# Performance work log

Measured on AMD Instinct MI355X. Metric: run time of the kernel, lower is better.

The kernel has to match this reference:

```python
import jax, jax.numpy as jnp
import numpy as np

DIM = 3072          # model dim
H = 24              # num heads (q == kv heads here)
DH = 128            # head dim
EPS = 1e-6
SCALE = 1.0 / float(np.sqrt(DH))
S_IMG, S_TXT, B = 2048, 256, 1


def _rmsnorm(x, w):
    # per-head RMSNorm over last (head_dim) axis
    return x * jax.lax.rsqrt(jnp.mean(x * x, axis=-1, keepdims=True) + EPS) * w


def _rope_non_neox(x, cos, sin):
    # x: [B,S,H,DH]; cos/sin: [S,DH/2]; interleaved (non-neox) rotation
    x1 = x[..., 0::2]
    x2 = x[..., 1::2]
    c = cos[None, :, None, :]
    s = sin[None, :, None, :]
    o1 = x1 * c - x2 * s
    o2 = x2 * c + x1 * s
    return jnp.stack([o1, o2], axis=-1).reshape(x.shape)


def setup_inputs() -> dict:
    key = jax.random.key(0)
    ks = jax.random.split(key, 16)
    hidden_states = jax.random.normal(ks[0], (B, S_IMG, DIM), jnp.float32)
    encoder_hidden_states = jax.random.normal(ks[1], (B, S_TXT, DIM), jnp.float32)
    vid_ang = jax.random.uniform(ks[2], (S_IMG, DH // 2), jnp.float32) * (2 * np.pi)
    txt_ang = jax.random.uniform(ks[3], (S_TXT, DH // 2), jnp.float32) * (2 * np.pi)
    w = 0.02
    return {
        "hidden_states": hidden_states,
        "encoder_hidden_states": encoder_hidden_states,
        "vid_cos": jnp.cos(vid_ang), "vid_sin": jnp.sin(vid_ang),
        "txt_cos": jnp.cos(txt_ang), "txt_sin": jnp.sin(txt_ang),
        "w_qkv": jax.random.normal(ks[4], (DIM, 3 * H * DH), jnp.float32) * w,
        "b_qkv": jnp.zeros((3 * H * DH,), jnp.float32),
        "w_add_qkv": jax.random.normal(ks[5], (DIM, 3 * H * DH), jnp.float32) * w,
        "b_add_qkv": jnp.zeros((3 * H * DH,), jnp.float32),
        "norm_q_w": jnp.ones((DH,), jnp.float32),
        "norm_k_w": jnp.ones((DH,), jnp.float32),
        "norm_aq_w": jnp.ones((DH,), jnp.float32),
        "norm_ak_w": jnp.ones((DH,), jnp.float32),
        "w_out": jax.random.normal(ks[6], (H * DH, DIM), jnp.float32) * w,
        "b_out": jnp.zeros((DIM,), jnp.float32),
        "w_add_out": jax.random.normal(ks[7], (H * DH, DIM), jnp.float32) * w,
        "b_add_out": jnp.zeros((DIM,), jnp.float32),
    }


def reference(hidden_states, encoder_hidden_states, vid_cos, vid_sin,
              txt_cos, txt_sin, w_qkv, b_qkv, w_add_qkv, b_add_qkv,
              norm_q_w, norm_k_w, norm_aq_w, norm_ak_w,
              w_out, b_out, w_add_out, b_add_out):
    qs = H * DH
    # fused QKV projections
    img_qkv = hidden_states @ w_qkv + b_qkv                  # [B,Si,3*H*DH]
    txt_qkv = encoder_hidden_states @ w_add_qkv + b_add_qkv  # [B,St,3*H*DH]

    def split_heads(qkv, S):
        q, k, v = qkv[..., :qs], qkv[..., qs:2 * qs], qkv[..., 2 * qs:]
        shp = (qkv.shape[0], S, H, DH)
        return q.reshape(shp), k.reshape(shp), v.reshape(shp)

    img_q, img_k, img_v = split_heads(img_qkv, S_IMG)
    txt_q, txt_k, txt_v = split_heads(txt_qkv, S_TXT)

    # per-head RMSNorm on q/k
    img_q = _rmsnorm(img_q, norm_q_w)
    img_k = _rmsnorm(img_k, norm_k_w)
    txt_q = _rmsnorm(txt_q, norm_aq_w)
    txt_k = _rmsnorm(txt_k, norm_ak_w)

    # non-neox RoPE on both query and key
    img_q = _rope_non_neox(img_q, vid_cos, vid_sin)
    img_k = _rope_non_neox(img_k, vid_cos, vid_sin)
    txt_q = _rope_non_neox(txt_q, txt_cos, txt_sin)
    txt_k = _rope_non_neox(txt_k, txt_cos, txt_sin)

    # joint text|image attention (text first), non-causal SDPA
    q = jnp.concatenate([txt_q, img_q], axis=1)  # [B,S,H,DH]
    k = jnp.concatenate([txt_k, img_k], axis=1)
    v = jnp.concatenate([txt_v, img_v], axis=1)

    scores = jnp.einsum('bqhd,bkhd->bhqk', q, k) * SCALE
    probs = jax.nn.softmax(scores, axis=-1)
    attn = jnp.einsum('bhqk,bkhd->bqhd', probs, v)           # [B,S,H,DH]
    attn = attn.reshape(attn.shape[0], attn.shape[1], H * DH)

    txt_attn = attn[:, :S_TXT, :]
    img_attn = attn[:, S_TXT:, :]
    img_out = img_attn @ w_out + b_out
    txt_out = txt_attn @ w_add_out + b_add_out
    return (img_out, txt_out)
```

## Files before the change

kernel.cpp:

```cpp
#include <hip/hip_runtime.h>

typedef unsigned short u16;
typedef __attribute__((ext_vector_type(8))) short bf16x8;
typedef __attribute__((ext_vector_type(4))) float f32x4;
typedef __attribute__((ext_vector_type(16))) float f32x16;

#define H_    24
#define DH_   128
#define DIM_  3072
#define NQKV_ 9216
#define SIMG_ 2048
#define STXT_ 256
#define SQ_   2304
#define SL_   0.1275258646912204f

__device__ __forceinline__ float bf2f(u16 h) {
  union { unsigned u; float f; } x; x.u = ((unsigned)h) << 16; return x.f;
}
__device__ __forceinline__ u16 f2bf(float f) {
  union { float f; unsigned u; } x; x.f = f;
  unsigned r = x.u + 0x7FFFu + ((x.u >> 16) & 1u);
  return (u16)(r >> 16);
}
__device__ __forceinline__ unsigned cvt_pk_bf16(float lo, float hi) {
  unsigned r;
  asm("v_cvt_pk_bf16_f32 %0, %1, %2" : "=v"(r) : "v"(lo), "v"(hi));
  return r;
}

__device__ __forceinline__ void gld16(const u16* g, u16* l) {
  __builtin_amdgcn_global_load_lds(
      (const __attribute__((address_space(1))) unsigned*)g,
      (__attribute__((address_space(3))) unsigned*)l, 16, 0, 0);
}

__global__ __launch_bounds__(256) void k_f2b2(const float* __restrict__ in0,
                                              u16* __restrict__ out0, int n0,
                                              const float* __restrict__ in1,
                                              u16* __restrict__ out1, int n1) {
  int i = (blockIdx.x * 256 + threadIdx.x) * 4;
  const float* in = in0;
  u16* out = out0;
  int n = n0;
  if (i >= n0) { i -= n0; in = in1; out = out1; n = n1; }
  if (i < n) {
    float4 v = *(const float4*)(in + i);
    ushort4 o;
    o.x = f2bf(v.x); o.y = f2bf(v.y); o.z = f2bf(v.z); o.w = f2bf(v.w);
    *(ushort4*)(out + i) = o;
  }
}

__global__ __launch_bounds__(256) void k_transpose2(const float* __restrict__ in0,
                                                    u16* __restrict__ out0,
                                                    const float* __restrict__ in1,
                                                    u16* __restrict__ out1,
                                                    int R, int C) {
  __shared__ __align__(16) u16 tile[64][72];
  const float* in = blockIdx.z ? in1 : in0;
  u16* out = blockIdx.z ? out1 : out0;
  const int t = threadIdx.x;
  const int tx = t & 15, ty = t >> 4;
  const int bc = blockIdx.x * 64, br = blockIdx.y * 64;
#pragma unroll
  for (int i = 0; i < 4; ++i) {
    const int r = ty + i * 16;
    float4 v = *(const float4*)(in + (size_t)(br + r) * C + bc + tx * 4);
    ushort4 o;
    o.x = f2bf(v.x); o.y = f2bf(v.y); o.z = f2bf(v.z); o.w = f2bf(v.w);
    *(ushort4*)&tile[r][tx * 4] = o;
  }
  __syncthreads();
#pragma unroll
  for (int i = 0; i < 4; ++i) {
    const int c = ty + i * 16;
    ushort4 v;
    v.x = tile[tx * 4 + 0][c];
    v.y = tile[tx * 4 + 1][c];
    v.z = tile[tx * 4 + 2][c];
    v.w = tile[tx * 4 + 3][c];
    *(ushort4*)(out + (size_t)(bc + c) * R + br + tx * 4) = v;
  }
}

template <bool F32OUT>
__global__ __launch_bounds__(256) void k_gemm_bt2(const u16* __restrict__ A0,
                                                  const u16* __restrict__ Bt0,
                                                  const float* __restrict__ bias0,
                                                  void* __restrict__ C0,
                                                  int M0,
                                                  const u16* __restrict__ A1,
                                                  const u16* __restrict__ Bt1,
                                                  const float* __restrict__ bias1,
                                                  void* __restrict__ C1,
                                                  int M1,
                                                  int N, int K, int nblk0) {
  __shared__ __align__(16) u16 As[2][128 * 32];
  __shared__ __align__(16) u16 Bs[2][128 * 32];
  const int t = threadIdx.x, w = t >> 6, l = t & 63;
  const int lr = l & 15, lg = l >> 4;
  const int wr = w >> 1, wc = w & 1;

  const u16 *A, *Bt;
  const float* bias;
  void* Cv;
  int M, wg, nwg;
  if ((int)blockIdx.x < nblk0) {
    A = A0; Bt = Bt0; bias = bias0; Cv = C0; M = M0;
    wg = blockIdx.x; nwg = nblk0;
  } else {
    A = A1; Bt = Bt1; bias = bias1; Cv = C1; M = M1;
    wg = blockIdx.x - nblk0; nwg = gridDim.x - nblk0;
  }
  const int nbm = M >> 7;
  if ((nwg & 7) == 0) {
    const int c = nwg >> 3;
    wg = (wg & 7) * c + (wg >> 3);
  }
  const int bm = (wg % nbm) * 128, bn = (wg / nbm) * 128;

  f32x4 acc[4][4];
#pragma unroll
  for (int i = 0; i < 4; ++i)
#pragma unroll
    for (int j = 0; j < 4; ++j) acc[i][j] = (f32x4){0.f, 0.f, 0.f, 0.f};

  const u16* Ag = A + (size_t)(bm + (t >> 2)) * K + (t & 3) * 8;
  const u16* Bg = Bt + (size_t)(bn + (t >> 2)) * K + (t & 3) * 8;

#define GSTAGE(buf)                                        \
  do {                                                     \
    gld16(Ag, &As[buf][t * 8]);                            \
    gld16(Ag + (size_t)64 * K, &As[buf][t * 8 + 2048]);    \
    gld16(Bg, &Bs[buf][t * 8]);                            \
    gld16(Bg + (size_t)64 * K, &Bs[buf][t * 8 + 2048]);    \
    Ag += 32; Bg += 32;                                    \
  } while (0)

  GSTAGE(0);
  const int nt = K >> 5;
  for (int tile = 0; tile < nt; ++tile) {
    const int cur = tile & 1;
    if (tile + 1 < nt) {
      GSTAGE(cur ^ 1);
      asm volatile("s_waitcnt vmcnt(4)" ::: "memory");
    } else {
      asm volatile("s_waitcnt vmcnt(0)" ::: "memory");
    }
    __builtin_amdgcn_s_barrier();
    bf16x8 af[4], bfr[4];
#pragma unroll
    for (int i = 0; i < 4; ++i)
      af[i] = *(const bf16x8*)&As[cur][(wr * 64 + i * 16 + lr) * 32 + lg * 8];
#pragma unroll
    for (int j = 0; j < 4; ++j)
      bfr[j] = *(const bf16x8*)&Bs[cur][(wc * 64 + j * 16 + lr) * 32 + lg * 8];
#pragma unroll
    for (int i = 0; i < 4; ++i)
#pragma unroll
      for (int j = 0; j < 4; ++j)
        acc[i][j] = __builtin_amdgcn_mfma_f32_16x16x32_bf16(af[i], bfr[j], acc[i][j], 0, 0, 0);
    __builtin_amdgcn_s_barrier();
  }
#undef GSTAGE

#pragma unroll
  for (int j = 0; j < 4; ++j) {
    const int col = bn + wc * 64 + j * 16 + lr;
    const float bv = bias[col];
#pragma unroll
    for (int i = 0; i < 4; ++i) {
      const int row = bm + wr * 64 + i * 16 + lg * 4;
#pragma unroll
      for (int r = 0; r < 4; ++r) {
        const float v = acc[i][j][r] + bv;
        if constexpr (F32OUT)
          ((float*)Cv)[(size_t)(row + r) * N + col] = v;
        else
          ((u16*)Cv)[(size_t)(row + r) * N + col] = f2bf(v);
      }
    }
  }
}

__global__ __launch_bounds__(256) void k_prep(
    const u16* __restrict__ img_qkv, const u16* __restrict__ txt_qkv,
    const float* __restrict__ vid_cos, const float* __restrict__ vid_sin,
    const float* __restrict__ txt_cos, const float* __restrict__ txt_sin,
    const float* __restrict__ nq, const float* __restrict__ nk,
    const float* __restrict__ naq, const float* __restrict__ nak,
    u16* __restrict__ Qb, u16* __restrict__ Kb, u16* __restrict__ Vt) {
  __shared__ __align__(16) u16 tile[64][136];
  const int t = threadIdx.x;
  if (blockIdx.x < (SQ_ / 64) * H_) {
    const int h = blockIdx.x / (SQ_ / 64), sb = blockIdx.x % (SQ_ / 64);
    {
      const int row = t >> 2, cc = (t & 3) * 32;
      const int s = sb * 64 + row;
      const u16* src = (s < STXT_) ? (txt_qkv + (size_t)s * NQKV_)
                                   : (img_qkv + (size_t)(s - STXT_) * NQKV_);
      src += 2 * DIM_ + h * DH_ + cc;
#pragma unroll
      for (int u = 0; u < 4; ++u) {
        uint4 a = *(const uint4*)(src + u * 8);
        *(uint4*)&tile[row][cc + u * 8] = a;
      }
    }
    __syncthreads();
    {
      const int w = t >> 6, lane = t & 63;
#pragma unroll 4
      for (int dd = 0; dd < 32; ++dd) {
        const int d = w * 32 + dd;
        const int m = (d & 7) << 3;
        const u16 v = tile[lane][d];
        Vt[((size_t)h * DH_ + d) * SQ_ + sb * 64 + (lane ^ m)] = v;
      }
    }
    return;
  }
  const int wid = (blockIdx.x - (SQ_ / 64) * H_) * 4 + (t >> 6);
  const int lane = t & 63;
  const int h = wid % H_, s = wid / H_;

  const u16* src;
  const float *cp, *sp, *qw, *kw;
  if (s < STXT_) {
    src = txt_qkv + (size_t)s * NQKV_;
    cp = txt_cos + s * 64; sp = txt_sin + s * 64;
    qw = naq; kw = nak;
  } else {
    const int si = s - STXT_;
    src = img_qkv + (size_t)si * NQKV_;
    cp = vid_cos + si * 64; sp = vid_sin + si * 64;
    qw = nq; kw = nk;
  }
  const float c = cp[lane], sn = sp[lane];
  const size_t drow = ((size_t)h * SQ_ + s) * DH_;

  {
    ushort2 p = *(const ushort2*)(src + h * DH_ + 2 * lane);
    float x1 = bf2f(p.x), x2 = bf2f(p.y);
    float ss = x1 * x1 + x2 * x2;
#pragma unroll
    for (int m = 1; m < 64; m <<= 1) ss += __shfl_xor(ss, m);
    const float rr = rsqrtf(ss * (1.0f / 128.0f) + 1e-6f);
    const float xn1 = x1 * rr * qw[2 * lane];
    const float xn2 = x2 * rr * qw[2 * lane + 1];
    ushort2 o; o.x = f2bf(xn1 * c - xn2 * sn); o.y = f2bf(xn2 * c + xn1 * sn);
    *(ushort2*)(Qb + drow + 2 * lane) = o;
  }
  {
    ushort2 p = *(const ushort2*)(src + DIM_ + h * DH_ + 2 * lane);
    float x1 = bf2f(p.x), x2 = bf2f(p.y);
    float ss = x1 * x1 + x2 * x2;
#pragma unroll
    for (int m = 1; m < 64; m <<= 1) ss += __shfl_xor(ss, m);
    const float rr = rsqrtf(ss * (1.0f / 128.0f) + 1e-6f);
    const float xn1 = x1 * rr * kw[2 * lane];
    const float xn2 = x2 * rr * kw[2 * lane + 1];
    ushort2 o; o.x = f2bf(xn1 * c - xn2 * sn); o.y = f2bf(xn2 * c + xn1 * sn);
    const int col = (2 * lane) ^ ((s & 7) << 3);
    *(ushort2*)(Kb + drow + col) = o;
  }
}

__global__ __launch_bounds__(256, 2) void k_attn(const u16* __restrict__ Qb,
                                                 const u16* __restrict__ Kb,
                                                 const u16* __restrict__ Vt,
                                                 u16* __restrict__ attnb) {
  __shared__ __align__(16) u16 Ks[2][64 * 128];
  __shared__ __align__(16) u16 Vs[2][128 * 64];
  const int t = threadIdx.x, w = t >> 6, l = t & 63;
  const int lo = l & 31, hi = l >> 5;

  const int bid = blockIdx.x;
  const int xcd = bid & 7, jj = bid >> 3;
  const int h = xcd * 3 + jj / 18;
  const int qb = jj % 18;

  const int q0 = qb * 128 + w * 32;
  const size_t head = (size_t)h * SQ_ * DH_;

  bf16x8 qf[8];
  {
    const u16* qp = Qb + head + (size_t)(q0 + lo) * DH_ + hi * 8;
#pragma unroll
    for (int ks = 0; ks < 8; ++ks) qf[ks] = *(const bf16x8*)(qp + ks * 16);
  }
  f32x16 oacc[4];
#pragma unroll
  for (int dt = 0; dt < 4; ++dt)
#pragma unroll
    for (int i = 0; i < 16; ++i) oacc[dt][i] = 0.f;
  float mrun = -1e30f, lrun = 0.f;

  const u16* kg0 = Kb + head + (size_t)(t >> 4) * DH_ + (t & 15) * 8;
  const u16* vg0 = Vt + head + (size_t)(t >> 3) * SQ_ + (t & 7) * 8;
  const int swz = (lo & 7) << 3;

#define STAGE(buf, kt)                                                   \
  do {                                                                   \
    const u16* kg_ = kg0 + (size_t)(kt) * 64 * DH_;                      \
    _Pragma("unroll")                                                    \
    for (int r_ = 0; r_ < 4; ++r_)                                       \
      gld16(kg_ + (size_t)r_ * 16 * DH_, &Ks[buf][t * 8 + r_ * 2048]);   \
    const u16* vg_ = vg0 + (kt) * 64;                                    \
    _Pragma("unroll")                                                    \
    for (int r_ = 0; r_ < 4; ++r_)                                       \
      gld16(vg_ + (size_t)r_ * 32 * SQ_, &Vs[buf][t * 8 + r_ * 2048]);   \
  } while (0)

  STAGE(0, 0);
  const int nt = SQ_ / 64;
  for (int kt = 0; kt < nt; ++kt) {
    const int cur = kt & 1;
    if (kt + 1 < nt) {
      STAGE(cur ^ 1, kt + 1);
      asm volatile("s_waitcnt vmcnt(8)" ::: "memory");
    } else {
      asm volatile("s_waitcnt vmcnt(0)" ::: "memory");
    }
    __builtin_amdgcn_s_barrier();

    f32x16 sv0, sv1;
#pragma unroll
    for (int i = 0; i < 16; ++i) { sv0[i] = 0.f; sv1[i] = 0.f; }
#pragma unroll
    for (int ks = 0; ks < 8; ++ks) {
      bf16x8 kf = *(const bf16x8*)&Ks[cur][lo * DH_ + ((ks * 16 + hi * 8) ^ swz)];
      sv0 = __builtin_amdgcn_mfma_f32_32x32x16_bf16(kf, qf[ks], sv0, 0, 0, 0);
    }
#pragma unroll
    for (int ks = 0; ks < 8; ++ks) {
      bf16x8 kf = *(const bf16x8*)&Ks[cur][(32 + lo) * DH_ + ((ks * 16 + hi * 8) ^ swz)];
      sv1 = __builtin_amdgcn_mfma_f32_32x32x16_bf16(kf, qf[ks], sv1, 0, 0, 0);
    }

    float tm = sv0[0];
#pragma unroll
    for (int i = 1; i < 16; ++i) tm = fmaxf(tm, sv0[i]);
#pragma unroll
    for (int i = 0; i < 16; ++i) tm = fmaxf(tm, sv1[i]);
    tm = fmaxf(tm, __shfl_xor(tm, 32));
    const float sc = tm * SL_;
    if (!__all(sc - mrun <= 8.0f)) {
      const float mn = fmaxf(mrun, sc);
      const float scl = __builtin_amdgcn_exp2f(mrun - mn);
      mrun = mn;
      lrun *= scl;
#pragma unroll
      for (int dt = 0; dt < 4; ++dt)
#pragma unroll
        for (int i = 0; i < 16; ++i) oacc[dt][i] *= scl;
    }
    float p0[16], p1[16];
    float rs = 0.f;
#pragma unroll
    for (int i = 0; i < 16; ++i) {
      p0[i] = __builtin_amdgcn_exp2f(fmaf(sv0[i], SL_, -mrun));
      rs += p0[i];
    }
#pragma unroll
    for (int i = 0; i < 16; ++i) {
      p1[i] = __builtin_amdgcn_exp2f(fmaf(sv1[i], SL_, -mrun));
      rs += p1[i];
    }
    rs += __shfl_xor(rs, 32);
    lrun += rs;

    unsigned xx[16];
#pragma unroll
    for (int g = 0; g < 8; ++g) xx[g] = cvt_pk_bf16(p0[2 * g], p0[2 * g + 1]);
#pragma unroll
    for (int g = 0; g < 8; ++g) xx[8 + g] = cvt_pk_bf16(p1[2 * g], p1[2 * g + 1]);
#pragma unroll
    for (int b = 0; b < 16; b += 4) {
      asm("v_permlane32_swap_b32 %0, %1" : "+v"(xx[b]), "+v"(xx[b + 2]));
      asm("v_permlane32_swap_b32 %0, %1" : "+v"(xx[b + 1]), "+v"(xx[b + 3]));
    }
    bf16x8 pb[4];
#pragma unroll
    for (int st = 0; st < 4; ++st) {
      union { unsigned u[4]; bf16x8 b; } cv;
      cv.u[0] = xx[4 * st]; cv.u[1] = xx[4 * st + 1];
      cv.u[2] = xx[4 * st + 2]; cv.u[3] = xx[4 * st + 3];
      pb[st] = cv.b;
    }

#pragma unroll
    for (int dt = 0; dt < 4; ++dt) {
      const int drow = dt * 32 + lo;
#pragma unroll
      for (int st = 0; st < 4; ++st) {
        bf16x8 vf = *(const bf16x8*)&Vs[cur][drow * 64 + ((st * 16 + hi * 8) ^ swz)];
        oacc[dt] = __builtin_amdgcn_mfma_f32_32x32x16_bf16(vf, pb[st], oacc[dt], 0, 0, 0);
      }
    }
    __builtin_amdgcn_s_barrier();
  }
#undef STAGE

  const float rinv = 1.0f / lrun;
  u16* op = attnb + (size_t)(q0 + lo) * DIM_ + h * DH_ + hi * 4;
#pragma unroll
  for (int dt = 0; dt < 4; ++dt)
#pragma unroll
    for (int g = 0; g < 4; ++g) {
      uint2 u;
      u.x = cvt_pk_bf16(oacc[dt][4 * g + 0] * rinv, oacc[dt][4 * g + 1] * rinv);
      u.y = cvt_pk_bf16(oacc[dt][4 * g + 2] * rinv, oacc[dt][4 * g + 3] * rinv);
      *(uint2*)(op + dt * 32 + g * 8) = u;
    }
}

extern "C" void kernel_launch(void* const* d_in, const int* in_sizes, int n_in,
                              void* d_out, int out_size, void* d_ws, size_t ws_size,
                              hipStream_t stream) {
  (void)in_sizes; (void)n_in; (void)out_size; (void)ws_size;
  const float* hidden    = (const float*)d_in[0];
  const float* encoder   = (const float*)d_in[1];
  const float* vid_cos   = (const float*)d_in[2];
  const float* vid_sin   = (const float*)d_in[3];
  const float* txt_cos   = (const float*)d_in[4];
  const float* txt_sin   = (const float*)d_in[5];
  const float* w_qkv     = (const float*)d_in[6];
  const float* b_qkv     = (const float*)d_in[7];
  const float* w_add_qkv = (const float*)d_in[8];
  const float* b_add_qkv = (const float*)d_in[9];
  const float* norm_q_w  = (const float*)d_in[10];
  const float* norm_k_w  = (const float*)d_in[11];
  const float* norm_aq_w = (const float*)d_in[12];
  const float* norm_ak_w = (const float*)d_in[13];
  const float* w_out     = (const float*)d_in[14];
  const float* b_out     = (const float*)d_in[15];
  const float* w_add_out = (const float*)d_in[16];
  const float* b_add_out = (const float*)d_in[17];
  float* out = (float*)d_out;

  char* ws = (char*)d_ws;
  u16* wqkv_t    = (u16*)(ws + 0);
  u16* waddqkv_t = (u16*)(ws + 56623104);
  u16* img_qkv   = (u16*)(ws + 113246208);
  u16* txt_qkv   = (u16*)(ws + 150994944);
  u16* Qb        = (u16*)(ws + 155713536);
  u16* Kb        = (u16*)(ws + 169869312);
  u16* Vt        = (u16*)(ws + 184025088);
  u16* wout_t    = wqkv_t;
  u16* waddout_t = waddqkv_t;
  u16* attnb     = img_qkv;
  u16* hidden_bf = Qb;
  u16* encoder_bf = Kb;

  k_f2b2<<<(SIMG_ * DIM_ + STXT_ * DIM_) / 1024, 256, 0, stream>>>(
      hidden, hidden_bf, SIMG_ * DIM_, encoder, encoder_bf, STXT_ * DIM_);
  k_transpose2<<<dim3(NQKV_ / 64, DIM_ / 64, 2), 256, 0, stream>>>(
      w_qkv, wqkv_t, w_add_qkv, waddqkv_t, DIM_, NQKV_);
  k_gemm_bt2<false><<<(SIMG_ / 128 + STXT_ / 128) * (NQKV_ / 128), 256, 0, stream>>>(
      hidden_bf, wqkv_t, b_qkv, img_qkv, SIMG_,
      encoder_bf, waddqkv_t, b_add_qkv, txt_qkv, STXT_,
      NQKV_, DIM_, (SIMG_ / 128) * (NQKV_ / 128));
  k_prep<<<(SQ_ / 64) * H_ + (SQ_ * H_) / 4, 256, 0, stream>>>(
      img_qkv, txt_qkv, vid_cos, vid_sin, txt_cos, txt_sin,
      norm_q_w, norm_k_w, norm_aq_w, norm_ak_w, Qb, Kb, Vt);
  k_attn<<<(SQ_ / 128) * H_, 256, 0, stream>>>(Qb, Kb, Vt, attnb);
  k_transpose2<<<dim3(DIM_ / 64, DIM_ / 64, 2), 256, 0, stream>>>(
      w_out, wout_t, w_add_out, waddout_t, DIM_, DIM_);
  k_gemm_bt2<true><<<(SIMG_ / 128 + STXT_ / 128) * (DIM_ / 128), 256, 0, stream>>>(
      attnb + (size_t)STXT_ * DIM_, wout_t, b_out, out, SIMG_,
      attnb, waddout_t, b_add_out, out + (size_t)SIMG_ * DIM_, STXT_,
      DIM_, DIM_, (SIMG_ / 128) * (DIM_ / 128));
}
```

Before: 438.6 us.

## Double GEMM K-tile to 64 with XOR-swizzled LDS layout

The bf16 GEMM main loop now stages a K-depth of 64 per iteration instead of 32, halving the number of barrier pairs and loop iterations, and each warp issues two MFMAs per accumulator per tile. The LDS layout uses an XOR swizzle on 16-byte chunks, both in the global-to-LDS copy and in the fragment reads, to avoid bank conflicts at the wider 128-byte row stride. Shared memory use doubles to 64 KB per block, which may reduce occupancy.

```diff
diff --git a/kernel.cpp b/kernel.cpp
--- a/kernel.cpp
+++ b/kernel.cpp
@@ -95,8 +95,8 @@
                                                   void* __restrict__ C1,
                                                   int M1,
                                                   int N, int K, int nblk0) {
-  __shared__ __align__(16) u16 As[2][128 * 32];
-  __shared__ __align__(16) u16 Bs[2][128 * 32];
+  __shared__ __align__(16) u16 As[2][128 * 64];
+  __shared__ __align__(16) u16 Bs[2][128 * 64];
   const int t = threadIdx.x, w = t >> 6, l = t & 63;
   const int lr = l & 15, lg = l >> 4;
   const int wr = w >> 1, wc = w & 1;
@@ -125,41 +125,57 @@
 #pragma unroll
     for (int j = 0; j < 4; ++j) acc[i][j] = (f32x4){0.f, 0.f, 0.f, 0.f};
 
-  const u16* Ag = A + (size_t)(bm + (t >> 2)) * K + (t & 3) * 8;
-  const u16* Bg = Bt + (size_t)(bn + (t >> 2)) * K + (t & 3) * 8;
-
-#define GSTAGE(buf)                                        \
-  do {                                                     \
-    gld16(Ag, &As[buf][t * 8]);                            \
-    gld16(Ag + (size_t)64 * K, &As[buf][t * 8 + 2048]);    \
-    gld16(Bg, &Bs[buf][t * 8]);                            \
-    gld16(Bg + (size_t)64 * K, &Bs[buf][t * 8 + 2048]);    \
-    Ag += 32; Bg += 32;                                    \
+  const int srow = t >> 3;
+  const int sgr = (t & 7) ^ (srow & 7);
+  const u16* Ag = A + (size_t)(bm + srow) * K + (sgr << 3);
+  const u16* Bg = Bt + (size_t)(bn + srow) * K + (sgr << 3);
+
+#define GSTAGE(buf, kt)                                                        \
+  do {                                                                         \
+    gld16(Ag + (kt) * 64,                       &As[buf][t * 8]);              \
+    gld16(Ag + (size_t)32 * K + (kt) * 64,      &As[buf][2048 + t * 8]);       \
+    gld16(Ag + (size_t)64 * K + (kt) * 64,      &As[buf][4096 + t * 8]);       \
+    gld16(Ag + (size_t)96 * K + (kt) * 64,      &As[buf][6144 + t * 8]);       \
+    gld16(Bg + (kt) * 64,                       &Bs[buf][t * 8]);              \
+    gld16(Bg + (size_t)32 * K + (kt) * 64,      &Bs[buf][2048 + t * 8]);       \
+    gld16(Bg + (size_t)64 * K + (kt) * 64,      &Bs[buf][4096 + t * 8]);       \
+    gld16(Bg + (size_t)96 * K + (kt) * 64,      &Bs[buf][6144 + t * 8]);       \
   } while (0)
 
-  GSTAGE(0);
-  const int nt = K >> 5;
+  GSTAGE(0, 0);
+  const int rsw = lr & 7;
+  const int kc0 = ((0 + lg) ^ rsw) << 3;
+  const int kc1 = ((4 + lg) ^ rsw) << 3;
+  const int nt = K >> 6;
   for (int tile = 0; tile < nt; ++tile) {
     const int cur = tile & 1;
     if (tile + 1 < nt) {
-      GSTAGE(cur ^ 1);
-      asm volatile("s_waitcnt vmcnt(4)" ::: "memory");
+      GSTAGE(cur ^ 1, tile + 1);
+      asm volatile("s_waitcnt vmcnt(8)" ::: "memory");
     } else {
       asm volatile("s_waitcnt vmcnt(0)" ::: "memory");
     }
     __builtin_amdgcn_s_barrier();
-    bf16x8 af[4], bfr[4];
+    bf16x8 af[4][2], bfr[4][2];
+#pragma unroll
+    for (int i = 0; i < 4; ++i) {
+      const int row = (wr * 64 + i * 16 + lr) * 64;
+      af[i][0] = *(const bf16x8*)&As[cur][row + kc0];
+      af[i][1] = *(const bf16x8*)&As[cur][row + kc1];
+    }
+#pragma unroll
+    for (int j = 0; j < 4; ++j) {
+      const int row = (wc * 64 + j * 16 + lr) * 64;
+      bfr[j][0] = *(const bf16x8*)&Bs[cur][row + kc0];
+      bfr[j][1] = *(const bf16x8*)&Bs[cur][row + kc1];
+    }
 #pragma unroll
     for (int i = 0; i < 4; ++i)
-      af[i] = *(const bf16x8*)&As[cur][(wr * 64 + i * 16 + lr) * 32 + lg * 8];
-#pragma unroll
-    for (int j = 0; j < 4; ++j)
-      bfr[j] = *(const bf16x8*)&Bs[cur][(wc * 64 + j * 16 + lr) * 32 + lg * 8];
-#pragma unroll
-    for (int i = 0; i < 4; ++i)
-#pragma unroll
-      for (int j = 0; j < 4; ++j)
-        acc[i][j] = __builtin_amdgcn_mfma_f32_16x16x32_bf16(af[i], bfr[j], acc[i][j], 0, 0, 0);
+#pragma unroll
+      for (int j = 0; j < 4; ++j) {
+        acc[i][j] = __builtin_amdgcn_mfma_f32_16x16x32_bf16(af[i][0], bfr[j][0], acc[i][j], 0, 0, 0);
+        acc[i][j] = __builtin_amdgcn_mfma_f32_16x16x32_bf16(af[i][1], bfr[j][1], acc[i][j], 0, 0, 0);
+      }
     __builtin_amdgcn_s_barrier();
   }
 #undef GSTAGE
```

Result: no change. 438.5 us (-0.0%).
